# Optimization experiments

Measured on AMD Instinct MI355X. Metric: run time of the kernel, lower is better.

Reference implementation:

```python
import jax, jax.numpy as jnp
import numpy as np

REG_PARAM = 0.05  # entropic regularisation (> 0 -> logsumexp branch)
N, M, D = 8192, 16384, 64


def setup_inputs() -> dict:
    key = jax.random.key(0)
    k1, k2 = jax.random.split(key)
    source_data = jax.random.normal(k1, (N, D), dtype=jnp.float32)
    target_data = jax.random.normal(k2, (M, D), dtype=jnp.float32)
    psi = jnp.zeros((M,), dtype=jnp.float32)
    return {"source_data": source_data, "target_data": target_data, "psi": psi}


def reference(source_data, target_data, psi):
    reg = jnp.float32(REG_PARAM)
    m = target_data.shape[0]
    # squared norms of target atoms, shape [M]; normalization = their mean
    sq_target = jnp.sum(target_data * target_data, axis=1)
    cost_norm = jnp.mean(sq_target)
    # pairwise squared distances [N, M], normalized
    sq_source = jnp.sum(source_data * source_data, axis=1, keepdims=True)  # [N,1]
    cross = jnp.matmul(source_data, target_data.T)                         # [N,M]
    cost_matrix = (sq_source + sq_target[None, :] - 2.0 * cross) / cost_norm
    # entropic semi-dual: mean(-reg * logsumexp((psi - C)/reg + log nu)) + mean(psi)
    log_nu = -jnp.log(jnp.float32(m))  # nu = uniform 1/M
    lse = jax.nn.logsumexp((psi[None, :] - cost_matrix) / reg + log_nu, axis=1)  # [N]
    return jnp.mean(-reg * lse) + jnp.mean(psi)
```

## Files before the change

kernel.cpp:

```cpp
#include <hip/hip_runtime.h>
#include <math.h>
#include <stdint.h>

#define N_SRC 8192
#define M_TGT 16384
#define DDIM  64
#define REG_P 0.05f
#define LOG2E 1.44269504088896340736f
#define LN2   0.69314718055994530942f

#define QSPLIT 8
#define CHUNKS (M_TGT / QSPLIT / 128)

typedef __attribute__((ext_vector_type(8))) short short8;
typedef __attribute__((ext_vector_type(4))) float f32x4;

#define OFF_TGT  0u
#define OFF_SRC  (2u << 20)
#define OFF_SQT  (3u << 20)
#define OFF_BIAS ((3u << 20) + 65536u)
#define OFF_A    ((3u << 20) + 131072u)
#define OFF_L    ((3u << 20) + 163840u)
#define OFF_SUMS ((3u << 20) + 196608u)

__device__ __forceinline__ unsigned short f2bf(float f) {
    unsigned u = __float_as_uint(f);
    u += 0x7fffu + ((u >> 16) & 1u);
    return (unsigned short)(u >> 16);
}

__device__ __forceinline__ float fast_exp2(float x) {
#if __has_builtin(__builtin_amdgcn_exp2f)
    return __builtin_amdgcn_exp2f(x);
#else
    return exp2f(x);
#endif
}

__device__ __forceinline__ void gload_lds16(const void* g, void* l) {
    __builtin_amdgcn_global_load_lds(
        (const __attribute__((address_space(1))) void*)g,
        (__attribute__((address_space(3))) void*)l, 16, 0, 0);
}

__global__ __launch_bounds__(256) void k1a_tgt(const float* __restrict__ tgt,
                                               const float* __restrict__ psi,
                                               char* __restrict__ ws) {
    const int tid = threadIdx.x;
    const int j   = blockIdx.x * 32 + (tid >> 3);
    const int d0  = (tid & 7) << 3;
    const float* rp = tgt + (size_t)j * DDIM + d0;
    float4 v0 = *(const float4*)rp;
    float4 v1 = *(const float4*)(rp + 4);
    short8 pk;
    pk[0]=(short)f2bf(v0.x); pk[1]=(short)f2bf(v0.y); pk[2]=(short)f2bf(v0.z); pk[3]=(short)f2bf(v0.w);
    pk[4]=(short)f2bf(v1.x); pk[5]=(short)f2bf(v1.y); pk[6]=(short)f2bf(v1.z); pk[7]=(short)f2bf(v1.w);
    const int c  = j >> 7, t = (j >> 4) & 7, lo = j & 15;
    const int kk = d0 >> 5, hi = (d0 >> 3) & 3;
    *(short8*)(ws + OFF_TGT + ((size_t)((c * 16 + t * 2 + kk) * 64 + hi * 16 + lo)) * 16) = pk;

    float sq = v0.x*v0.x + v0.y*v0.y + v0.z*v0.z + v0.w*v0.w
             + v1.x*v1.x + v1.y*v1.y + v1.z*v1.z + v1.w*v1.w;
    float rs = sq;
    rs += __shfl_xor(rs, 1); rs += __shfl_xor(rs, 2); rs += __shfl_xor(rs, 4);
    if ((tid & 7) == 0) ((float*)(ws + OFF_SQT))[j] = rs;
    float ps = ((tid & 7) == 0) ? psi[j] : 0.f;

    __shared__ float r0[256], r1[256];
    r0[tid] = sq; r1[tid] = ps;
    __syncthreads();
    for (int off = 128; off > 0; off >>= 1) {
        if (tid < off) { r0[tid] += r0[tid + off]; r1[tid] += r1[tid + off]; }
        __syncthreads();
    }
    if (tid == 0) {
        float* sums = (float*)(ws + OFF_SUMS);
        atomicAdd(&sums[0], r0[0]);
        atomicAdd(&sums[1], r1[0]);
    }
}

__global__ __launch_bounds__(256) void k1b_src(const float* __restrict__ src,
                                               const float* __restrict__ psi,
                                               char* __restrict__ ws) {
    const int tid = threadIdx.x;
    const float* sums = (const float*)(ws + OFF_SUMS);
    const float inv_cn = (float)M_TGT / sums[0];
    if (blockIdx.x < 256) {
        const int i  = blockIdx.x * 32 + (tid >> 3);
        const int d0 = (tid & 7) << 3;
        const float* rp = src + (size_t)i * DDIM + d0;
        float4 v0 = *(const float4*)rp;
        float4 v1 = *(const float4*)(rp + 4);
        short8 pk;
        pk[0]=(short)f2bf(v0.x); pk[1]=(short)f2bf(v0.y); pk[2]=(short)f2bf(v0.z); pk[3]=(short)f2bf(v0.w);
        pk[4]=(short)f2bf(v1.x); pk[5]=(short)f2bf(v1.y); pk[6]=(short)f2bf(v1.z); pk[7]=(short)f2bf(v1.w);
        const int g = i >> 4, lo = i & 15;
        const int kk = d0 >> 5, hi = (d0 >> 3) & 3;
        *(short8*)(ws + OFF_SRC + ((size_t)((g * 2 + kk) * 64 + hi * 16 + lo)) * 16) = pk;
        float sq = v0.x*v0.x + v0.y*v0.y + v0.z*v0.z + v0.w*v0.w
                 + v1.x*v1.x + v1.y*v1.y + v1.z*v1.z + v1.w*v1.w;
        float rs = sq;
        rs += __shfl_xor(rs, 1); rs += __shfl_xor(rs, 2); rs += __shfl_xor(rs, 4);
        if ((tid & 7) == 0)
            ((float*)(ws + OFF_A))[i] = -rs * inv_cn * (1.0f / REG_P) - logf((float)M_TGT);
    } else {
        const int j = (blockIdx.x - 256) * 256 + tid;
        const float sqt = ((const float*)(ws + OFF_SQT))[j];
        ((float*)(ws + OFF_BIAS))[j] = (psi[j] - sqt * inv_cn) * (1.0f / REG_P) * LOG2E;
    }
}

__global__ __launch_bounds__(256, 4) void k2_main(char* __restrict__ ws) {
    const int tid  = threadIdx.x;
    const int lane = tid & 63;
    const int w    = tid >> 6;
    const int rowblk = blockIdx.x >> 3;
    const int q      = blockIdx.x & (QSPLIT - 1);
    const int row0   = rowblk * 64;

    __shared__ __align__(16) char s_buf[2][16384];
    __shared__ float s_bias[2][128];

    const float* sums = (const float*)(ws + OFF_SUMS);
    const float inv_cn = (float)M_TGT / sums[0];
    const float alpha2 = 2.0f * inv_cn * (1.0f / REG_P) * LOG2E;

    const short8* __restrict__ srcst = (const short8*)(ws + OFF_SRC);
    short8 Af[4][2];
#pragma unroll
    for (int g = 0; g < 4; ++g)
#pragma unroll
        for (int kk = 0; kk < 2; ++kk)
            Af[g][kk] = srcst[((row0 >> 4) + g) * 128 + kk * 64 + lane];

    const float* __restrict__ biasArr = (const float*)(ws + OFF_BIAS);

    float lsum[4][4];
#pragma unroll
    for (int g = 0; g < 4; ++g)
#pragma unroll
        for (int r = 0; r < 4; ++r) lsum[g][r] = 0.f;

    {
        const int gc = q * CHUNKS;
        const char* gp = ws + OFF_TGT + (size_t)gc * 16384;
#pragma unroll
        for (int r = 0; r < 4; ++r)
            gload_lds16(gp + (r * 256 + tid) * 16, &s_buf[0][(r * 256 + (tid & ~63)) * 16]);
        if (tid < 128) s_bias[0][tid] = biasArr[gc * 128 + tid];
    }

    for (int c = 0; c < CHUNKS; ++c) {
        __syncthreads();
        if (c + 1 < CHUNKS) {
            const int gc = q * CHUNKS + c + 1;
            const char* gp = ws + OFF_TGT + (size_t)gc * 16384;
            const int nb = (c + 1) & 1;
#pragma unroll
            for (int r = 0; r < 4; ++r)
                gload_lds16(gp + (r * 256 + tid) * 16, &s_buf[nb][(r * 256 + (tid & ~63)) * 16]);
            if (tid < 128) s_bias[nb][tid] = biasArr[gc * 128 + tid];
        }
        const char* buf = s_buf[c & 1];
        const float* bias = s_bias[c & 1];
#pragma unroll
        for (int s = 0; s < 2; ++s) {
            const int t = w + s * 4;
            short8 B0 = *(const short8*)(buf + ((t * 2 + 0) * 64 + lane) * 16);
            short8 B1 = *(const short8*)(buf + ((t * 2 + 1) * 64 + lane) * 16);
            const float bt = bias[t * 16 + (lane & 15)];
            f32x4 acc[4];
#pragma unroll
            for (int g = 0; g < 4; ++g) {
                f32x4 a = {0.f, 0.f, 0.f, 0.f};
                a = __builtin_amdgcn_mfma_f32_16x16x32_bf16(Af[g][0], B0, a, 0, 0, 0);
                a = __builtin_amdgcn_mfma_f32_16x16x32_bf16(Af[g][1], B1, a, 0, 0, 0);
                acc[g] = a;
            }
#pragma unroll
            for (int g = 0; g < 4; ++g)
#pragma unroll
                for (int r = 0; r < 4; ++r)
                    lsum[g][r] += fast_exp2(fmaf(alpha2, acc[g][r], bt));
        }
    }

    float* ws_l = (float*)(ws + OFF_L);
#pragma unroll
    for (int g = 0; g < 4; ++g)
#pragma unroll
        for (int r = 0; r < 4; ++r) {
            float v = lsum[g][r];
            v += __shfl_xor(v, 1); v += __shfl_xor(v, 2);
            v += __shfl_xor(v, 4); v += __shfl_xor(v, 8);
            if ((lane & 15) == 0)
                atomicAdd(&ws_l[row0 + g * 16 + (lane >> 4) * 4 + r], v);
        }
}

__global__ __launch_bounds__(256) void k3_final(const char* __restrict__ ws,
                                                float* __restrict__ out) {
    const int tid = threadIdx.x;
    const float* A = (const float*)(ws + OFF_A);
    const float* L = (const float*)(ws + OFF_L);
    const float* sums = (const float*)(ws + OFF_SUMS);
    float acc = 0.f;
    for (int i = tid; i < N_SRC; i += 256)
        acc += -REG_P * (A[i] + LN2 * __log2f(L[i]));
    __shared__ float red[256];
    red[tid] = acc;
    __syncthreads();
    for (int off = 128; off > 0; off >>= 1) {
        if (tid < off) red[tid] += red[tid + off];
        __syncthreads();
    }
    if (tid == 0)
        out[0] = red[0] / (float)N_SRC + sums[1] / (float)M_TGT;
}

extern "C" void kernel_launch(void* const* d_in, const int* in_sizes, int n_in,
                              void* d_out, int out_size, void* d_ws, size_t ws_size,
                              hipStream_t stream) {
    const float* src = (const float*)d_in[0];
    const float* tgt = (const float*)d_in[1];
    const float* psi = (const float*)d_in[2];
    char* ws = (char*)d_ws;

    hipMemsetAsync(ws + OFF_L, 0, 32768 + 64, stream);

    k1a_tgt<<<M_TGT / 32, 256, 0, stream>>>(tgt, psi, ws);
    k1b_src<<<256 + M_TGT / 256, 256, 0, stream>>>(src, psi, ws);
    k2_main<<<(N_SRC / 64) * QSPLIT, 256, 0, stream>>>(ws);
    k3_final<<<1, 256, 0, stream>>>(ws, (float*)d_out);
}
```

Before: 119.0 us.

## Merge preprocessing kernels, drop memset and atomics, stream B from global

Fuses the target and source bf16 staging kernels into one launch that writes per-block partial sums instead of atomics, which removes the memset and one launch. The main kernel now reduces those partials itself, computes the per-column bias inline from psi and sqt, and has each wave load its own B fragments straight from global memory with register prefetch instead of LDS double buffering. Row sums go to per-split slots and are combined in the final kernel, so no atomics are needed. This removes launch and synchronisation overhead but relies on L2 serving the B tiles without LDS sharing between waves.

```diff
diff --git a/kernel.cpp b/kernel.cpp
--- a/kernel.cpp
+++ b/kernel.cpp
@@ -8,9 +8,7 @@
 #define REG_P 0.05f
 #define LOG2E 1.44269504088896340736f
 #define LN2   0.69314718055994530942f
-
 #define QSPLIT 8
-#define CHUNKS (M_TGT / QSPLIT / 128)
 
 typedef __attribute__((ext_vector_type(8))) short short8;
 typedef __attribute__((ext_vector_type(4))) float f32x4;
@@ -18,10 +16,11 @@
 #define OFF_TGT  0u
 #define OFF_SRC  (2u << 20)
 #define OFF_SQT  (3u << 20)
-#define OFF_BIAS ((3u << 20) + 65536u)
-#define OFF_A    ((3u << 20) + 131072u)
-#define OFF_L    ((3u << 20) + 163840u)
-#define OFF_SUMS ((3u << 20) + 196608u)
+#define OFF_SQS  ((3u << 20) + 65536u)
+#define OFF_PART ((3u << 20) + 98304u)
+#define OFF_L    ((3u << 20) + 102400u)
+
+#define K1_BLOCKS 384
 
 __device__ __forceinline__ unsigned short f2bf(float f) {
     unsigned u = __float_as_uint(f);
@@ -37,94 +36,100 @@
 #endif
 }
 
-__device__ __forceinline__ void gload_lds16(const void* g, void* l) {
-    __builtin_amdgcn_global_load_lds(
-        (const __attribute__((address_space(1))) void*)g,
-        (__attribute__((address_space(3))) void*)l, 16, 0, 0);
-}
-
-__global__ __launch_bounds__(256) void k1a_tgt(const float* __restrict__ tgt,
-                                               const float* __restrict__ psi,
-                                               char* __restrict__ ws) {
-    const int tid = threadIdx.x;
-    const int j   = blockIdx.x * 32 + (tid >> 3);
-    const int d0  = (tid & 7) << 3;
-    const float* rp = tgt + (size_t)j * DDIM + d0;
-    float4 v0 = *(const float4*)rp;
-    float4 v1 = *(const float4*)(rp + 4);
-    short8 pk;
-    pk[0]=(short)f2bf(v0.x); pk[1]=(short)f2bf(v0.y); pk[2]=(short)f2bf(v0.z); pk[3]=(short)f2bf(v0.w);
-    pk[4]=(short)f2bf(v1.x); pk[5]=(short)f2bf(v1.y); pk[6]=(short)f2bf(v1.z); pk[7]=(short)f2bf(v1.w);
-    const int c  = j >> 7, t = (j >> 4) & 7, lo = j & 15;
-    const int kk = d0 >> 5, hi = (d0 >> 3) & 3;
-    *(short8*)(ws + OFF_TGT + ((size_t)((c * 16 + t * 2 + kk) * 64 + hi * 16 + lo)) * 16) = pk;
-
-    float sq = v0.x*v0.x + v0.y*v0.y + v0.z*v0.z + v0.w*v0.w
-             + v1.x*v1.x + v1.y*v1.y + v1.z*v1.z + v1.w*v1.w;
-    float rs = sq;
-    rs += __shfl_xor(rs, 1); rs += __shfl_xor(rs, 2); rs += __shfl_xor(rs, 4);
-    if ((tid & 7) == 0) ((float*)(ws + OFF_SQT))[j] = rs;
-    float ps = ((tid & 7) == 0) ? psi[j] : 0.f;
-
-    __shared__ float r0[256], r1[256];
-    r0[tid] = sq; r1[tid] = ps;
+__global__ __launch_bounds__(256) void k1_stage(const float* __restrict__ src,
+                                                const float* __restrict__ tgt,
+                                                const float* __restrict__ psi,
+                                                char* __restrict__ ws) {
+    const int tid  = threadIdx.x;
+    const int wave = tid >> 6;
+    const int lane = tid & 63;
+    const int lo   = lane & 15;
+    const int hi   = lane >> 4;
+    const int task = blockIdx.x * 4 + wave;
+
+    float sq_contrib = 0.f;
+    float ps_contrib = 0.f;
+
+    if (task < 1024) {
+        const int T = task;
+        const int j = T * 16 + lo;
+        float sq = 0.f;
+#pragma unroll
+        for (int kk = 0; kk < 2; ++kk) {
+            const float* p = tgt + (size_t)j * DDIM + kk * 32 + hi * 8;
+            float4 v0 = ((const float4*)p)[0];
+            float4 v1 = ((const float4*)p)[1];
+            short8 pk;
+            pk[0]=(short)f2bf(v0.x); pk[1]=(short)f2bf(v0.y); pk[2]=(short)f2bf(v0.z); pk[3]=(short)f2bf(v0.w);
+            pk[4]=(short)f2bf(v1.x); pk[5]=(short)f2bf(v1.y); pk[6]=(short)f2bf(v1.z); pk[7]=(short)f2bf(v1.w);
+            ((short8*)(ws + OFF_TGT))[(T * 2 + kk) * 64 + lane] = pk;
+            sq += v0.x*v0.x + v0.y*v0.y + v0.z*v0.z + v0.w*v0.w
+                + v1.x*v1.x + v1.y*v1.y + v1.z*v1.z + v1.w*v1.w;
+        }
+        float r = sq;
+        r += __shfl_xor(r, 16); r += __shfl_xor(r, 32);
+        if (hi == 0) {
+            ((float*)(ws + OFF_SQT))[j] = r;
+            ps_contrib = psi[j];
+        }
+        sq_contrib = sq;
+    } else {
+        const int g = task - 1024;
+        const int i = g * 16 + lo;
+        float sq = 0.f;
+#pragma unroll
+        for (int kk = 0; kk < 2; ++kk) {
+            const float* p = src + (size_t)i * DDIM + kk * 32 + hi * 8;
+            float4 v0 = ((const float4*)p)[0];
+            float4 v1 = ((const float4*)p)[1];
+            short8 pk;
+            pk[0]=(short)f2bf(v0.x); pk[1]=(short)f2bf(v0.y); pk[2]=(short)f2bf(v0.z); pk[3]=(short)f2bf(v0.w);
+            pk[4]=(short)f2bf(v1.x); pk[5]=(short)f2bf(v1.y); pk[6]=(short)f2bf(v1.z); pk[7]=(short)f2bf(v1.w);
+            ((short8*)(ws + OFF_SRC))[(g * 2 + kk) * 64 + lane] = pk;
+            sq += v0.x*v0.x + v0.y*v0.y + v0.z*v0.z + v0.w*v0.w
+                + v1.x*v1.x + v1.y*v1.y + v1.z*v1.z + v1.w*v1.w;
+        }
+        float r = sq;
+        r += __shfl_xor(r, 16); r += __shfl_xor(r, 32);
+        if (hi == 0) ((float*)(ws + OFF_SQS))[i] = r;
+    }
+
+    float a = sq_contrib, b = ps_contrib;
+#pragma unroll
+    for (int off = 1; off < 64; off <<= 1) {
+        a += __shfl_xor(a, off);
+        b += __shfl_xor(b, off);
+    }
+    __shared__ float s_a[4], s_b[4];
+    if (lane == 0) { s_a[wave] = a; s_b[wave] = b; }
     __syncthreads();
-    for (int off = 128; off > 0; off >>= 1) {
-        if (tid < off) { r0[tid] += r0[tid + off]; r1[tid] += r1[tid + off]; }
-        __syncthreads();
-    }
     if (tid == 0) {
-        float* sums = (float*)(ws + OFF_SUMS);
-        atomicAdd(&sums[0], r0[0]);
-        atomicAdd(&sums[1], r1[0]);
-    }
-}
-
-__global__ __launch_bounds__(256) void k1b_src(const float* __restrict__ src,
-                                               const float* __restrict__ psi,
-                                               char* __restrict__ ws) {
-    const int tid = threadIdx.x;
-    const float* sums = (const float*)(ws + OFF_SUMS);
-    const float inv_cn = (float)M_TGT / sums[0];
-    if (blockIdx.x < 256) {
-        const int i  = blockIdx.x * 32 + (tid >> 3);
-        const int d0 = (tid & 7) << 3;
-        const float* rp = src + (size_t)i * DDIM + d0;
-        float4 v0 = *(const float4*)rp;
-        float4 v1 = *(const float4*)(rp + 4);
-        short8 pk;
-        pk[0]=(short)f2bf(v0.x); pk[1]=(short)f2bf(v0.y); pk[2]=(short)f2bf(v0.z); pk[3]=(short)f2bf(v0.w);
-        pk[4]=(short)f2bf(v1.x); pk[5]=(short)f2bf(v1.y); pk[6]=(short)f2bf(v1.z); pk[7]=(short)f2bf(v1.w);
-        const int g = i >> 4, lo = i & 15;
-        const int kk = d0 >> 5, hi = (d0 >> 3) & 3;
-        *(short8*)(ws + OFF_SRC + ((size_t)((g * 2 + kk) * 64 + hi * 16 + lo)) * 16) = pk;
-        float sq = v0.x*v0.x + v0.y*v0.y + v0.z*v0.z + v0.w*v0.w
-                 + v1.x*v1.x + v1.y*v1.y + v1.z*v1.z + v1.w*v1.w;
-        float rs = sq;
-        rs += __shfl_xor(rs, 1); rs += __shfl_xor(rs, 2); rs += __shfl_xor(rs, 4);
-        if ((tid & 7) == 0)
-            ((float*)(ws + OFF_A))[i] = -rs * inv_cn * (1.0f / REG_P) - logf((float)M_TGT);
-    } else {
-        const int j = (blockIdx.x - 256) * 256 + tid;
-        const float sqt = ((const float*)(ws + OFF_SQT))[j];
-        ((float*)(ws + OFF_BIAS))[j] = (psi[j] - sqt * inv_cn) * (1.0f / REG_P) * LOG2E;
-    }
-}
-
-__global__ __launch_bounds__(256, 4) void k2_main(char* __restrict__ ws) {
-    const int tid  = threadIdx.x;
-    const int lane = tid & 63;
-    const int w    = tid >> 6;
+        float2 out;
+        out.x = s_a[0] + s_a[1] + s_a[2] + s_a[3];
+        out.y = s_b[0] + s_b[1] + s_b[2] + s_b[3];
+        ((float2*)(ws + OFF_PART))[blockIdx.x] = out;
+    }
+}
+
+__global__ __launch_bounds__(256, 4) void k2_main(const float* __restrict__ psi,
+                                                  char* __restrict__ ws) {
+    const int tid    = threadIdx.x;
+    const int lane   = tid & 63;
+    const int w      = tid >> 6;
     const int rowblk = blockIdx.x >> 3;
     const int q      = blockIdx.x & (QSPLIT - 1);
     const int row0   = rowblk * 64;
 
-    __shared__ __align__(16) char s_buf[2][16384];
-    __shared__ float s_bias[2][128];
-
-    const float* sums = (const float*)(ws + OFF_SUMS);
-    const float inv_cn = (float)M_TGT / sums[0];
-    const float alpha2 = 2.0f * inv_cn * (1.0f / REG_P) * LOG2E;
+    const float2* __restrict__ part = (const float2*)(ws + OFF_PART);
+    float ssq = 0.f;
+#pragma unroll
+    for (int k = 0; k < K1_BLOCKS / 64; ++k) ssq += part[k * 64 + lane].x;
+#pragma unroll
+    for (int off = 1; off < 64; off <<= 1) ssq += __shfl_xor(ssq, off);
+    const float inv_cn = (float)M_TGT / ssq;
+    const float c_psi  = (1.0f / REG_P) * LOG2E;
+    const float c_sqt  = inv_cn * c_psi;
+    const float alpha2 = 2.0f * c_sqt;
 
     const short8* __restrict__ srcst = (const short8*)(ws + OFF_SRC);
     short8 Af[4][2];
@@ -134,7 +139,11 @@
         for (int kk = 0; kk < 2; ++kk)
             Af[g][kk] = srcst[((row0 >> 4) + g) * 128 + kk * 64 + lane];
 
-    const float* __restrict__ biasArr = (const float*)(ws + OFF_BIAS);
+    const short8* __restrict__ tgtst = (const short8*)(ws + OFF_TGT);
+    const float*  __restrict__ sqt   = (const float*)(ws + OFF_SQT);
+
+    const int T0    = (q * 2048 + w * 512) >> 4;
+    const int jlane = (T0 << 4) + (lane & 15);
 
     float lsum[4][4];
 #pragma unroll
@@ -142,51 +151,38 @@
 #pragma unroll
         for (int r = 0; r < 4; ++r) lsum[g][r] = 0.f;
 
-    {
-        const int gc = q * CHUNKS;
-        const char* gp = ws + OFF_TGT + (size_t)gc * 16384;
-#pragma unroll
-        for (int r = 0; r < 4; ++r)
-            gload_lds16(gp + (r * 256 + tid) * 16, &s_buf[0][(r * 256 + (tid & ~63)) * 16]);
-        if (tid < 128) s_bias[0][tid] = biasArr[gc * 128 + tid];
-    }
-
-    for (int c = 0; c < CHUNKS; ++c) {
-        __syncthreads();
-        if (c + 1 < CHUNKS) {
-            const int gc = q * CHUNKS + c + 1;
-            const char* gp = ws + OFF_TGT + (size_t)gc * 16384;
-            const int nb = (c + 1) & 1;
+    short8 B0n = tgtst[(T0 * 2 + 0) * 64 + lane];
+    short8 B1n = tgtst[(T0 * 2 + 1) * 64 + lane];
+    float  psn = psi[jlane];
+    float  sqn = sqt[jlane];
+
+    for (int t = 0; t < 32; ++t) {
+        short8 B0 = B0n, B1 = B1n;
+        float  ps = psn, sq = sqn;
+        if (t < 31) {
+            const int Tg = T0 + t + 1;
+            B0n = tgtst[(Tg * 2 + 0) * 64 + lane];
+            B1n = tgtst[(Tg * 2 + 1) * 64 + lane];
+            psn = psi[jlane + (t + 1) * 16];
+            sqn = sqt[jlane + (t + 1) * 16];
+        }
+        const float bias = ps * c_psi - sq * c_sqt;
+        f32x4 acc[4];
+#pragma unroll
+        for (int g = 0; g < 4; ++g) {
+            f32x4 a = {0.f, 0.f, 0.f, 0.f};
+            a = __builtin_amdgcn_mfma_f32_16x16x32_bf16(Af[g][0], B0, a, 0, 0, 0);
+            a = __builtin_amdgcn_mfma_f32_16x16x32_bf16(Af[g][1], B1, a, 0, 0, 0);
+            acc[g] = a;
+        }
+#pragma unroll
+        for (int g = 0; g < 4; ++g)
 #pragma unroll
             for (int r = 0; r < 4; ++r)
-                gload_lds16(gp + (r * 256 + tid) * 16, &s_buf[nb][(r * 256 + (tid & ~63)) * 16]);
-            if (tid < 128) s_bias[nb][tid] = biasArr[gc * 128 + tid];
-        }
-        const char* buf = s_buf[c & 1];
-        const float* bias = s_bias[c & 1];
-#pragma unroll
-        for (int s = 0; s < 2; ++s) {
-            const int t = w + s * 4;
-            short8 B0 = *(const short8*)(buf + ((t * 2 + 0) * 64 + lane) * 16);
-            short8 B1 = *(const short8*)(buf + ((t * 2 + 1) * 64 + lane) * 16);
-            const float bt = bias[t * 16 + (lane & 15)];
-            f32x4 acc[4];
-#pragma unroll
-            for (int g = 0; g < 4; ++g) {
-                f32x4 a = {0.f, 0.f, 0.f, 0.f};
-                a = __builtin_amdgcn_mfma_f32_16x16x32_bf16(Af[g][0], B0, a, 0, 0, 0);
-                a = __builtin_amdgcn_mfma_f32_16x16x32_bf16(Af[g][1], B1, a, 0, 0, 0);
-                acc[g] = a;
-            }
-#pragma unroll
-            for (int g = 0; g < 4; ++g)
-#pragma unroll
-                for (int r = 0; r < 4; ++r)
-                    lsum[g][r] += fast_exp2(fmaf(alpha2, acc[g][r], bt));
-        }
-    }
-
-    float* ws_l = (float*)(ws + OFF_L);
+                lsum[g][r] += fast_exp2(fmaf(alpha2, acc[g][r], bias));
+    }
+
+    __shared__ float s_l[4][64];
 #pragma unroll
     for (int g = 0; g < 4; ++g)
 #pragma unroll
@@ -195,28 +191,55 @@
             v += __shfl_xor(v, 1); v += __shfl_xor(v, 2);
             v += __shfl_xor(v, 4); v += __shfl_xor(v, 8);
             if ((lane & 15) == 0)
-                atomicAdd(&ws_l[row0 + g * 16 + (lane >> 4) * 4 + r], v);
-        }
-}
-
-__global__ __launch_bounds__(256) void k3_final(const char* __restrict__ ws,
-                                                float* __restrict__ out) {
-    const int tid = threadIdx.x;
-    const float* A = (const float*)(ws + OFF_A);
-    const float* L = (const float*)(ws + OFF_L);
-    const float* sums = (const float*)(ws + OFF_SUMS);
+                s_l[w][g * 16 + (lane >> 4) * 4 + r] = v;
+        }
+    __syncthreads();
+    if (tid < 64) {
+        float v = s_l[0][tid] + s_l[1][tid] + s_l[2][tid] + s_l[3][tid];
+        ((float*)(ws + OFF_L))[q * N_SRC + row0 + tid] = v;
+    }
+}
+
+__global__ __launch_bounds__(1024) void k3_final(const char* __restrict__ ws,
+                                                 float* __restrict__ out) {
+    const int tid  = threadIdx.x;
+    const int lane = tid & 63;
+
+    const float2* __restrict__ part = (const float2*)(ws + OFF_PART);
+    float ssq = 0.f, spsi = 0.f;
+#pragma unroll
+    for (int k = 0; k < K1_BLOCKS / 64; ++k) {
+        float2 p = part[k * 64 + lane];
+        ssq += p.x; spsi += p.y;
+    }
+#pragma unroll
+    for (int off = 1; off < 64; off <<= 1) {
+        ssq  += __shfl_xor(ssq, off);
+        spsi += __shfl_xor(spsi, off);
+    }
+    const float inv_cn = (float)M_TGT / ssq;
+
+    const float* __restrict__ L   = (const float*)(ws + OFF_L);
+    const float* __restrict__ sqs = (const float*)(ws + OFF_SQS);
+    const float logM = logf((float)M_TGT);
+
     float acc = 0.f;
-    for (int i = tid; i < N_SRC; i += 256)
-        acc += -REG_P * (A[i] + LN2 * __log2f(L[i]));
-    __shared__ float red[256];
+    for (int i = tid; i < N_SRC; i += 1024) {
+        float lt = 0.f;
+#pragma unroll
+        for (int qq = 0; qq < QSPLIT; ++qq) lt += L[qq * N_SRC + i];
+        const float A = -sqs[i] * inv_cn * (1.0f / REG_P) - logM;
+        acc += -REG_P * (A + LN2 * __log2f(lt));
+    }
+    __shared__ float red[1024];
     red[tid] = acc;
     __syncthreads();
-    for (int off = 128; off > 0; off >>= 1) {
+    for (int off = 512; off > 0; off >>= 1) {
         if (tid < off) red[tid] += red[tid + off];
         __syncthreads();
     }
     if (tid == 0)
-        out[0] = red[0] / (float)N_SRC + sums[1] / (float)M_TGT;
+        out[0] = red[0] / (float)N_SRC + spsi / (float)M_TGT;
 }
 
 extern "C" void kernel_launch(void* const* d_in, const int* in_sizes, int n_in,
@@ -227,10 +250,7 @@
     const float* psi = (const float*)d_in[2];
     char* ws = (char*)d_ws;
 
-    hipMemsetAsync(ws + OFF_L, 0, 32768 + 64, stream);
-
-    k1a_tgt<<<M_TGT / 32, 256, 0, stream>>>(tgt, psi, ws);
-    k1b_src<<<256 + M_TGT / 256, 256, 0, stream>>>(src, psi, ws);
-    k2_main<<<(N_SRC / 64) * QSPLIT, 256, 0, stream>>>(ws);
-    k3_final<<<1, 256, 0, stream>>>(ws, (float*)d_out);
-}
+    k1_stage<<<K1_BLOCKS, 256, 0, stream>>>(src, tgt, psi, ws);
+    k2_main<<<(N_SRC / 64) * QSPLIT, 256, 0, stream>>>(psi, ws);
+    k3_final<<<1, 1024, 0, stream>>>(ws, (float*)d_out);
+}
```

Result: faster. 101.0 us (-15.1%).
